# Performance work log

Measured on AMD Instinct MI355X. Metric: run time of the kernel, lower is better.

## Reference

```python
import jax, jax.numpy as jnp
import numpy as np

ALPHA = 0.5
SIGMA = 0.1
EPS = 1e-8
NUM_RISKS, B, T = 2, 8192, 64


def setup_inputs() -> dict:
    key = jax.random.key(0)
    k1, k2, k3, k4 = jax.random.split(key, 4)
    risk_outputs = jax.random.uniform(k1, (NUM_RISKS, B, T), dtype=jnp.float32)
    time_bins = jax.random.randint(k2, (B,), 0, T, dtype=jnp.int64)
    risk_indicators = jax.random.randint(k3, (B, NUM_RISKS), 0, 2).astype(bool)
    event_indicators = jax.random.randint(k4, (B,), 0, 2).astype(bool)
    return {
        "risk_outputs": risk_outputs,
        "time_bins": time_bins,
        "risk_indicators": risk_indicators,
        "event_indicators": event_indicators,
    }


def _deephit_loss(risk_outputs, time_bins, risk_indicators, event_indicators):
    ev = event_indicators  # (B,) bool: event occurred
    cens = ~ev             # (B,) bool: censored
    # pairwise mask M[i,j]: i censored, j had event, t_j <= t_i
    pair_mask = cens[:, None] & ev[None, :] & (time_bins[None, :] <= time_bins[:, None])

    def per_risk(pred, rind):
        # pred: (B, T), rind: (B,) bool
        # ---- likelihood: -mean(log p_i(t_i)) over samples with this risk's event
        probs = jnp.take_along_axis(pred, time_bins[:, None], axis=1)[:, 0]  # (B,)
        mask = rind & ev
        cnt = mask.sum()
        log_sum = jnp.where(mask, jnp.log(probs + EPS), 0.0).sum()
        ll = jnp.where(cnt > 0, -log_sum / jnp.maximum(cnt, 1).astype(pred.dtype), 0.0)
        # ---- ranking: sum sigmoid((F_i(t_i) - F_j(t_i)) / sigma) over valid (i,j) pairs
        cum = jnp.cumsum(pred, axis=1)          # (B, T)
        G = cum[:, time_bins].T                  # G[i, j] = cum[j, t_i]  -> (B, B)
        diff = jnp.diagonal(G)[:, None] - G      # cum[i,t_i] - cum[j,t_i]
        rl = jnp.where(pair_mask, jax.nn.sigmoid(diff / SIGMA), 0.0).sum()
        return ll, rl

    ll, rl = jax.vmap(per_risk)(risk_outputs, risk_indicators.T)
    return ALPHA * ll.sum() + (1.0 - ALPHA) * rl.sum()


def reference(risk_outputs, time_bins, risk_indicators, event_indicators):
    return _deephit_loss(risk_outputs, time_bins, risk_indicators, event_indicators)
```

## Files before the change

kernel.cpp:

```cpp
#include <hip/hip_runtime.h>
#include <math.h>


namespace {
constexpr int R  = 2;
constexpr int Bn = 8192;
constexpr int Tn = 64;
constexpr float INV_SIGMA = 10.0f;
constexpr float EPS       = 1e-8f;
}


__global__ void k_prep(const int* __restrict__ tb, const int* __restrict__ ev,
                       int* limE, int* cbase, int* ncensG,
                       int* esort, int* csort, int* accZero) {
    __shared__ int hE[Tn], hC[Tn], wE[Tn], wC[Tn];
    int tid = threadIdx.x;
    if (tid < Tn) { hE[tid] = 0; hC[tid] = 0; }
    if (tid < 192) accZero[tid] = 0;
    __syncthreads();
    for (int j = tid; j < Bn; j += 1024) {
        int t = tb[j];
        if (ev[j]) atomicAdd(&hE[t], 1);
        else       atomicAdd(&hC[t], 1);
    }
    __syncthreads();
    if (tid == 0) {
        int ae = 0, ac = 0;
        for (int t = 0; t < Tn; ++t) {
            wE[t] = ae; ae += hE[t]; limE[t] = ae;
            wC[t] = ac; cbase[t] = ac; ncensG[t] = hC[t]; ac += hC[t];
        }
    }
    __syncthreads();
    for (int j = tid; j < Bn; j += 1024) {
        int t = tb[j];
        if (ev[j]) { int p = atomicAdd(&wE[t], 1); esort[p] = j; }
        else       { int p = atomicAdd(&wC[t], 1); csort[p] = j; }
    }
}

__global__ void __launch_bounds__(256)
k_cum(const float* __restrict__ risk, const int* __restrict__ tb,
      const int* __restrict__ rind,
      const int* __restrict__ limE, const int* __restrict__ cbase,
      const int* __restrict__ ncens,
      const int* __restrict__ esort, const int* __restrict__ csort,
      float* __restrict__ cumTs, float* __restrict__ aCens,
      float* llsumArr, int* cntArr) {
    const int r    = blockIdx.y;
    const int lane = threadIdx.x & 63;
    const int w    = threadIdx.x >> 6;
    __shared__ float S[Tn][Tn + 1];
    __shared__ int idxS[Tn];

    if (blockIdx.x < 128) {
        int nE = limE[Tn - 1];
        int k0 = blockIdx.x * 64;
        if (k0 >= nE) return;
        int cnt = min(64, nE - k0);
        if (threadIdx.x < cnt) idxS[threadIdx.x] = esort[k0 + threadIdx.x];
        __syncthreads();
        for (int s = 0; s < 16; ++s) {
            int ls = w * 16 + s;
            if (ls < cnt) {
                int i = idxS[ls];
                float v = risk[((size_t)r * Bn + i) * Tn + lane];
                float c = v;
#pragma unroll
                for (int o = 1; o < 64; o <<= 1) {
                    float u = __shfl_up(c, o, 64);
                    if (lane >= o) c += u;
                }
                S[lane][ls] = c;
                int ti = tb[i];
                float p = __shfl(v, ti, 64);
                if (lane == 0 && rind[i * R + r]) {
                    int slot = r * 32 + ((k0 + ls) & 31);
                    atomicAdd(&llsumArr[slot], logf(p + EPS));
                    atomicAdd(&cntArr[slot], 1);
                }
            }
        }
        __syncthreads();
        float* dst = cumTs + ((size_t)r * Tn) * Bn + k0;
        int col = threadIdx.x & 63;
        int tr0 = threadIdx.x >> 6;
        if (col < cnt) {
#pragma unroll
            for (int m = 0; m < 16; ++m) {
                int t = m * 4 + tr0;
                dst[(size_t)t * Bn + col] = S[t][col];
            }
        }
    } else {
        int nC = cbase[Tn - 1] + ncens[Tn - 1];
        int k0 = (blockIdx.x - 128) * 64;
        if (k0 >= nC) return;
        int cnt = min(64, nC - k0);
        if (threadIdx.x < cnt) idxS[threadIdx.x] = csort[k0 + threadIdx.x];
        __syncthreads();
        for (int s = 0; s < 16; ++s) {
            int ls = w * 16 + s;
            if (ls < cnt) {
                int i  = idxS[ls];
                int ti = tb[i];
                float v = risk[((size_t)r * Bn + i) * Tn + lane];
                v = (lane <= ti) ? v : 0.f;
#pragma unroll
                for (int o = 32; o > 0; o >>= 1) v += __shfl_down(v, o, 64);
                if (lane == 0) aCens[r * Bn + k0 + ls] = v;
            }
        }
    }
}

__global__ void k_rank(const float* __restrict__ cumTs, const float* __restrict__ aCens,
                       const int* __restrict__ limE, const int* __restrict__ cbase,
                       const int* __restrict__ ncens, float* rlsumArr) {
    int t = blockIdx.z, r = blockIdx.y, ec = blockIdx.x;
    int ne = limE[t];
    if (ec * 1024 >= ne) return;
    int nc = ncens[t];
    if (nc == 0) return;

    int j0 = ec * 1024 + threadIdx.x * 4;
    const float* rowp = cumTs + ((size_t)(r * Tn + t)) * Bn;
    float4 c4 = *reinterpret_cast<const float4*>(rowp + j0);
    float c0 = (j0 + 0 < ne) ? c4.x * INV_SIGMA : INFINITY;
    float c1 = (j0 + 1 < ne) ? c4.y * INV_SIGMA : INFINITY;
    float c2 = (j0 + 2 < ne) ? c4.z * INV_SIGMA : INFINITY;
    float c3 = (j0 + 3 < ne) ? c4.w * INV_SIGMA : INFINITY;

    const float* aC = aCens + r * Bn + cbase[t];
    float s0 = 0.f, s1 = 0.f, s2 = 0.f, s3 = 0.f;
#pragma unroll 4
    for (int ii = 0; ii < nc; ++ii) {
        float a10 = aC[ii] * INV_SIGMA;
        s0 += __builtin_amdgcn_rcpf(1.f + __expf(c0 - a10));
        s1 += __builtin_amdgcn_rcpf(1.f + __expf(c1 - a10));
        s2 += __builtin_amdgcn_rcpf(1.f + __expf(c2 - a10));
        s3 += __builtin_amdgcn_rcpf(1.f + __expf(c3 - a10));
    }
    float s = (s0 + s1) + (s2 + s3);
#pragma unroll
    for (int o = 32; o > 0; o >>= 1) s += __shfl_down(s, o, 64);
    if ((threadIdx.x & 63) == 0) {
        int slot = r * 32 + ((blockIdx.z * 8 + blockIdx.x) & 31);
        atomicAdd(&rlsumArr[slot], s);
    }
}

__global__ void k_final(const float* llsumArr, const int* cntArr,
                        const float* rlsumArr, float* out) {
    int lane = threadIdx.x;
    float lg = llsumArr[lane];
    float rl = rlsumArr[lane];
    int   cn = cntArr[lane];
#pragma unroll
    for (int o = 1; o <= 16; o <<= 1) {
        lg += __shfl_xor(lg, o, 64);
        rl += __shfl_xor(rl, o, 64);
        cn += __shfl_xor(cn, o, 64);
    }
    float lg1 = __shfl(lg, 32, 64);
    float rl1 = __shfl(rl, 32, 64);
    int   cn1 = __shfl(cn, 32, 64);
    if (lane == 0) {
        float ll0 = (cn  > 0) ? (-lg  / (float)cn ) : 0.f;
        float ll1 = (cn1 > 0) ? (-lg1 / (float)cn1) : 0.f;
        out[0] = 0.5f * (ll0 + ll1) + 0.5f * (rl + rl1);
    }
}

extern "C" void kernel_launch(void* const* d_in, const int* in_sizes, int n_in,
                              void* d_out, int out_size, void* d_ws, size_t ws_size,
                              hipStream_t stream) {
    const float* risk = (const float*)d_in[0];
    const int* tb     = (const int*)d_in[1];
    const int* rind   = (const int*)d_in[2];
    const int* ev     = (const int*)d_in[3];

    char* ws = (char*)d_ws;
    float* llsumArr = (float*)(ws + 0);
    int*   cntArr   = (int*)(ws + 256);
    float* rlsumArr = (float*)(ws + 512);
    int*   limE     = (int*)(ws + 768);
    int*   cbase    = (int*)(ws + 1024);
    int*   ncens    = (int*)(ws + 1280);
    int*   esort    = (int*)(ws + 2048);
    int*   csort    = (int*)(ws + 34816);
    float* aCens    = (float*)(ws + 67584);
    float* cumTs    = (float*)(ws + 133120);

    k_prep<<<1, 1024, 0, stream>>>(tb, ev, limE, cbase, ncens, esort, csort,
                                   (int*)ws);
    dim3 gc(256, R);
    k_cum<<<gc, 256, 0, stream>>>(risk, tb, rind, limE, cbase, ncens,
                                  esort, csort, cumTs, aCens, llsumArr, cntArr);
    dim3 gr(8, R, Tn);
    k_rank<<<gr, 256, 0, stream>>>(cumTs, aCens, limE, cbase, ncens, rlsumArr);
    k_final<<<1, 64, 0, stream>>>(llsumArr, cntArr, rlsumArr, (float*)d_out);
}
```

Before: 116.8 us.

## Fuse all stages into one persistent kernel with software grid barriers

Replaces the four-kernel pipeline with a single persistent 256-block, 1024-thread kernel that uses atomic grid barriers between the histogram, scan, scatter, cumulative-sum and ranking stages. The histogram and scatter are now spread over 8 blocks instead of one, and the ranking work is split by (risk, time, half of the censored range) across all blocks. This targets launch overhead and the serial single-block prep kernel. In exchange it adds grid-barrier spin costs and a memset launch, and it relies on all 256 large blocks being co-resident, which can deadlock if that does not hold.

```diff
diff --git a/kernel.cpp b/kernel.cpp
--- a/kernel.cpp
+++ b/kernel.cpp
@@ -6,170 +6,228 @@
 constexpr int R  = 2;
 constexpr int Bn = 8192;
 constexpr int Tn = 64;
+constexpr int NB = 256;
+constexpr int NT = 1024;
 constexpr float INV_SIGMA = 10.0f;
 constexpr float EPS       = 1e-8f;
 }
 
 
-__global__ void k_prep(const int* __restrict__ tb, const int* __restrict__ ev,
-                       int* limE, int* cbase, int* ncensG,
-                       int* esort, int* csort, int* accZero) {
-    __shared__ int hE[Tn], hC[Tn], wE[Tn], wC[Tn];
-    int tid = threadIdx.x;
-    if (tid < Tn) { hE[tid] = 0; hC[tid] = 0; }
-    if (tid < 192) accZero[tid] = 0;
+__device__ __forceinline__ void gridbar(int* bar, int want) {
     __syncthreads();
-    for (int j = tid; j < Bn; j += 1024) {
+    if (threadIdx.x == 0) {
+        __threadfence();
+        int t = __hip_atomic_fetch_add(&bar[0], 1, __ATOMIC_ACQ_REL,
+                                       __HIP_MEMORY_SCOPE_AGENT);
+        if (t == NB - 1) {
+            __hip_atomic_store(&bar[0], 0, __ATOMIC_RELAXED,
+                               __HIP_MEMORY_SCOPE_AGENT);
+            __hip_atomic_fetch_add(&bar[1], 1, __ATOMIC_ACQ_REL,
+                                   __HIP_MEMORY_SCOPE_AGENT);
+        } else {
+            while (__hip_atomic_load(&bar[1], __ATOMIC_ACQUIRE,
+                                     __HIP_MEMORY_SCOPE_AGENT) < want) {
+                __builtin_amdgcn_s_sleep(2);
+            }
+        }
+        __threadfence();
+    }
+    __syncthreads();
+}
+
+__global__ void __launch_bounds__(NT)
+k_fused(const float* __restrict__ risk, const int* __restrict__ tb,
+        const int* __restrict__ rind, const int* __restrict__ ev,
+        float* __restrict__ out, int* __restrict__ wsI) {
+    float* llsumArr = (float*)(wsI + 0);
+    int*   cntArr   = wsI + 64;
+    float* rlsumArr = (float*)(wsI + 128);
+    int*   bar      = wsI + 192;
+    int*   binE     = wsI + 208;
+    int*   binC     = wsI + 272;
+    int*   limE     = wsI + 336;
+    int*   cbaseA   = wsI + 400;
+    int*   ncensA   = wsI + 464;
+    int*   scatE    = wsI + 528;
+    int*   scatC    = wsI + 592;
+    int*   esort    = wsI + 1024;
+    int*   csort    = wsI + 9216;
+    float* aCens    = (float*)(wsI + 17408);
+    float* cumTs    = (float*)(wsI + 33792);
+
+    const int b    = blockIdx.x;
+    const int tid  = threadIdx.x;
+    const int lane = tid & 63;
+    const int w    = tid >> 6;
+
+    __shared__ float S[Tn][Tn + 1];
+    __shared__ int idxS[Tn], tbS[Tn];
+    __shared__ int hE[Tn], hC[Tn];
+
+    if (b < 8) {
+        if (tid < Tn) { hE[tid] = 0; hC[tid] = 0; }
+        __syncthreads();
+        int j = b * 1024 + tid;
         int t = tb[j];
         if (ev[j]) atomicAdd(&hE[t], 1);
         else       atomicAdd(&hC[t], 1);
-    }
-    __syncthreads();
-    if (tid == 0) {
-        int ae = 0, ac = 0;
-        for (int t = 0; t < Tn; ++t) {
-            wE[t] = ae; ae += hE[t]; limE[t] = ae;
-            wC[t] = ac; cbase[t] = ac; ncensG[t] = hC[t]; ac += hC[t];
-        }
-    }
-    __syncthreads();
-    for (int j = tid; j < Bn; j += 1024) {
+        __syncthreads();
+        if (tid < Tn) {
+            if (hE[tid]) atomicAdd(&binE[tid], hE[tid]);
+            if (hC[tid]) atomicAdd(&binC[tid], hC[tid]);
+        }
+    }
+    gridbar(bar, 1);
+
+    if (b == 0 && tid < 64) {
+        int eC = binE[tid], cC = binC[tid];
+        int se = eC, sc = cC;
+#pragma unroll
+        for (int o = 1; o < 64; o <<= 1) {
+            int ue = __shfl_up(se, o, 64);
+            int uc = __shfl_up(sc, o, 64);
+            if (lane >= o) { se += ue; sc += uc; }
+        }
+        limE[tid]   = se;
+        scatE[tid]  = se - eC;
+        cbaseA[tid] = sc - cC;
+        scatC[tid]  = sc - cC;
+        ncensA[tid] = cC;
+    }
+    gridbar(bar, 2);
+
+    if (b < 8) {
+        int j = b * 1024 + tid;
         int t = tb[j];
-        if (ev[j]) { int p = atomicAdd(&wE[t], 1); esort[p] = j; }
-        else       { int p = atomicAdd(&wC[t], 1); csort[p] = j; }
-    }
-}
-
-__global__ void __launch_bounds__(256)
-k_cum(const float* __restrict__ risk, const int* __restrict__ tb,
-      const int* __restrict__ rind,
-      const int* __restrict__ limE, const int* __restrict__ cbase,
-      const int* __restrict__ ncens,
-      const int* __restrict__ esort, const int* __restrict__ csort,
-      float* __restrict__ cumTs, float* __restrict__ aCens,
-      float* llsumArr, int* cntArr) {
-    const int r    = blockIdx.y;
-    const int lane = threadIdx.x & 63;
-    const int w    = threadIdx.x >> 6;
-    __shared__ float S[Tn][Tn + 1];
-    __shared__ int idxS[Tn];
-
-    if (blockIdx.x < 128) {
-        int nE = limE[Tn - 1];
-        int k0 = blockIdx.x * 64;
-        if (k0 >= nE) return;
-        int cnt = min(64, nE - k0);
-        if (threadIdx.x < cnt) idxS[threadIdx.x] = esort[k0 + threadIdx.x];
-        __syncthreads();
-        for (int s = 0; s < 16; ++s) {
-            int ls = w * 16 + s;
-            if (ls < cnt) {
-                int i = idxS[ls];
-                float v = risk[((size_t)r * Bn + i) * Tn + lane];
-                float c = v;
-#pragma unroll
-                for (int o = 1; o < 64; o <<= 1) {
-                    float u = __shfl_up(c, o, 64);
-                    if (lane >= o) c += u;
+        if (ev[j]) { int p = atomicAdd(&scatE[t], 1); esort[p] = j; }
+        else       { int p = atomicAdd(&scatC[t], 1); csort[p] = j; }
+    }
+    gridbar(bar, 3);
+
+    int nE = limE[Tn - 1];
+    int nC = Bn - nE;
+    for (int c = b; c < 512; c += NB) {
+        bool isEvent = (c < 256);
+        int r  = (c >> 7) & 1;
+        int k0 = (c & 127) * 64;
+        int tot = isEvent ? nE : nC;
+        if (k0 < tot) {
+            int cnt = min(64, tot - k0);
+            if (tid < cnt) {
+                int i = isEvent ? esort[k0 + tid] : csort[k0 + tid];
+                idxS[tid] = i;
+                tbS[tid]  = tb[i];
+            }
+            __syncthreads();
+            if (isEvent) {
+#pragma unroll
+                for (int s = 0; s < 4; ++s) {
+                    int ls = s * 16 + w;
+                    if (ls < cnt) {
+                        int i = idxS[ls];
+                        float v = risk[((size_t)r * Bn + i) * Tn + lane];
+                        float cc = v;
+#pragma unroll
+                        for (int o = 1; o < 64; o <<= 1) {
+                            float u = __shfl_up(cc, o, 64);
+                            if (lane >= o) cc += u;
+                        }
+                        S[lane][ls] = cc;
+                        int ti = tbS[ls];
+                        float p = __shfl(v, ti, 64);
+                        if (lane == 0 && rind[i * R + r]) {
+                            int slot = r * 32 + ((k0 + ls) & 31);
+                            atomicAdd(&llsumArr[slot], logf(p + EPS));
+                            atomicAdd(&cntArr[slot], 1);
+                        }
+                    }
                 }
-                S[lane][ls] = c;
-                int ti = tb[i];
-                float p = __shfl(v, ti, 64);
-                if (lane == 0 && rind[i * R + r]) {
-                    int slot = r * 32 + ((k0 + ls) & 31);
-                    atomicAdd(&llsumArr[slot], logf(p + EPS));
-                    atomicAdd(&cntArr[slot], 1);
+                __syncthreads();
+                int col = tid & 63, tr0 = tid >> 6;
+                if (col < cnt) {
+                    float* dst = cumTs + ((size_t)r * Tn) * Bn + k0;
+#pragma unroll
+                    for (int m = 0; m < 4; ++m) {
+                        int t = m * 16 + tr0;
+                        dst[(size_t)t * Bn + col] = S[t][col];
+                    }
                 }
-            }
-        }
-        __syncthreads();
-        float* dst = cumTs + ((size_t)r * Tn) * Bn + k0;
-        int col = threadIdx.x & 63;
-        int tr0 = threadIdx.x >> 6;
-        if (col < cnt) {
-#pragma unroll
-            for (int m = 0; m < 16; ++m) {
-                int t = m * 4 + tr0;
-                dst[(size_t)t * Bn + col] = S[t][col];
-            }
-        }
-    } else {
-        int nC = cbase[Tn - 1] + ncens[Tn - 1];
-        int k0 = (blockIdx.x - 128) * 64;
-        if (k0 >= nC) return;
-        int cnt = min(64, nC - k0);
-        if (threadIdx.x < cnt) idxS[threadIdx.x] = csort[k0 + threadIdx.x];
-        __syncthreads();
-        for (int s = 0; s < 16; ++s) {
-            int ls = w * 16 + s;
-            if (ls < cnt) {
-                int i  = idxS[ls];
-                int ti = tb[i];
-                float v = risk[((size_t)r * Bn + i) * Tn + lane];
-                v = (lane <= ti) ? v : 0.f;
-#pragma unroll
-                for (int o = 32; o > 0; o >>= 1) v += __shfl_down(v, o, 64);
-                if (lane == 0) aCens[r * Bn + k0 + ls] = v;
-            }
-        }
-    }
-}
-
-__global__ void k_rank(const float* __restrict__ cumTs, const float* __restrict__ aCens,
-                       const int* __restrict__ limE, const int* __restrict__ cbase,
-                       const int* __restrict__ ncens, float* rlsumArr) {
-    int t = blockIdx.z, r = blockIdx.y, ec = blockIdx.x;
-    int ne = limE[t];
-    if (ec * 1024 >= ne) return;
-    int nc = ncens[t];
-    if (nc == 0) return;
-
-    int j0 = ec * 1024 + threadIdx.x * 4;
-    const float* rowp = cumTs + ((size_t)(r * Tn + t)) * Bn;
-    float4 c4 = *reinterpret_cast<const float4*>(rowp + j0);
-    float c0 = (j0 + 0 < ne) ? c4.x * INV_SIGMA : INFINITY;
-    float c1 = (j0 + 1 < ne) ? c4.y * INV_SIGMA : INFINITY;
-    float c2 = (j0 + 2 < ne) ? c4.z * INV_SIGMA : INFINITY;
-    float c3 = (j0 + 3 < ne) ? c4.w * INV_SIGMA : INFINITY;
-
-    const float* aC = aCens + r * Bn + cbase[t];
-    float s0 = 0.f, s1 = 0.f, s2 = 0.f, s3 = 0.f;
+                __syncthreads();
+            } else {
+#pragma unroll
+                for (int s = 0; s < 4; ++s) {
+                    int ls = s * 16 + w;
+                    if (ls < cnt) {
+                        int i  = idxS[ls];
+                        int ti = tbS[ls];
+                        float v = risk[((size_t)r * Bn + i) * Tn + lane];
+                        v = (lane <= ti) ? v : 0.f;
+#pragma unroll
+                        for (int o = 32; o > 0; o >>= 1) v += __shfl_down(v, o, 64);
+                        if (lane == 0) aCens[r * Bn + k0 + ls] = v;
+                    }
+                }
+                __syncthreads();
+            }
+        }
+    }
+    gridbar(bar, 4);
+
+    {
+        int r    = b >> 7;
+        int t    = (b >> 1) & 63;
+        int half = b & 1;
+        int ne = limE[t], nc = ncensA[t], cb = cbaseA[t];
+        float s = 0.f;
+        if (ne > 0 && nc > 0) {
+            int e0 = tid * 4;
+            const float* rowp = cumTs + ((size_t)(r * Tn + t)) * Bn;
+            float4 c4 = *reinterpret_cast<const float4*>(rowp + e0);
+            float c0 = (e0 + 0 < ne) ? c4.x * INV_SIGMA : INFINITY;
+            float c1 = (e0 + 1 < ne) ? c4.y * INV_SIGMA : INFINITY;
+            float c2 = (e0 + 2 < ne) ? c4.z * INV_SIGMA : INFINITY;
+            float c3 = (e0 + 3 < ne) ? c4.w * INV_SIGMA : INFINITY;
+            int lo = half ? (nc >> 1) : 0;
+            int hi = half ? nc : (nc >> 1);
+            const float* aC = aCens + r * Bn + cb;
+            float s0 = 0.f, s1 = 0.f, s2 = 0.f, s3 = 0.f;
 #pragma unroll 4
-    for (int ii = 0; ii < nc; ++ii) {
-        float a10 = aC[ii] * INV_SIGMA;
-        s0 += __builtin_amdgcn_rcpf(1.f + __expf(c0 - a10));
-        s1 += __builtin_amdgcn_rcpf(1.f + __expf(c1 - a10));
-        s2 += __builtin_amdgcn_rcpf(1.f + __expf(c2 - a10));
-        s3 += __builtin_amdgcn_rcpf(1.f + __expf(c3 - a10));
-    }
-    float s = (s0 + s1) + (s2 + s3);
-#pragma unroll
-    for (int o = 32; o > 0; o >>= 1) s += __shfl_down(s, o, 64);
-    if ((threadIdx.x & 63) == 0) {
-        int slot = r * 32 + ((blockIdx.z * 8 + blockIdx.x) & 31);
-        atomicAdd(&rlsumArr[slot], s);
-    }
-}
-
-__global__ void k_final(const float* llsumArr, const int* cntArr,
-                        const float* rlsumArr, float* out) {
-    int lane = threadIdx.x;
-    float lg = llsumArr[lane];
-    float rl = rlsumArr[lane];
-    int   cn = cntArr[lane];
-#pragma unroll
-    for (int o = 1; o <= 16; o <<= 1) {
-        lg += __shfl_xor(lg, o, 64);
-        rl += __shfl_xor(rl, o, 64);
-        cn += __shfl_xor(cn, o, 64);
-    }
-    float lg1 = __shfl(lg, 32, 64);
-    float rl1 = __shfl(rl, 32, 64);
-    int   cn1 = __shfl(cn, 32, 64);
-    if (lane == 0) {
-        float ll0 = (cn  > 0) ? (-lg  / (float)cn ) : 0.f;
-        float ll1 = (cn1 > 0) ? (-lg1 / (float)cn1) : 0.f;
-        out[0] = 0.5f * (ll0 + ll1) + 0.5f * (rl + rl1);
+            for (int ci = lo; ci < hi; ++ci) {
+                float a10 = aC[ci] * INV_SIGMA;
+                s0 += __builtin_amdgcn_rcpf(1.f + __expf(c0 - a10));
+                s1 += __builtin_amdgcn_rcpf(1.f + __expf(c1 - a10));
+                s2 += __builtin_amdgcn_rcpf(1.f + __expf(c2 - a10));
+                s3 += __builtin_amdgcn_rcpf(1.f + __expf(c3 - a10));
+            }
+            s = (s0 + s1) + (s2 + s3);
+        }
+#pragma unroll
+        for (int o = 32; o > 0; o >>= 1) s += __shfl_down(s, o, 64);
+        if (lane == 0) {
+            int r2 = b >> 7;
+            atomicAdd(&rlsumArr[r2 * 32 + ((b * 16 + w) & 31)], s);
+        }
+    }
+    gridbar(bar, 5);
+
+    if (b == 0 && tid < 64) {
+        float lg = llsumArr[tid];
+        float rl = rlsumArr[tid];
+        int   cn = cntArr[tid];
+#pragma unroll
+        for (int o = 1; o <= 16; o <<= 1) {
+            lg += __shfl_xor(lg, o, 64);
+            rl += __shfl_xor(rl, o, 64);
+            cn += __shfl_xor(cn, o, 64);
+        }
+        float lg1 = __shfl(lg, 32, 64);
+        float rl1 = __shfl(rl, 32, 64);
+        int   cn1 = __shfl(cn, 32, 64);
+        if (tid == 0) {
+            float ll0 = (cn  > 0) ? (-lg  / (float)cn ) : 0.f;
+            float ll1 = (cn1 > 0) ? (-lg1 / (float)cn1) : 0.f;
+            out[0] = 0.5f * (ll0 + ll1) + 0.5f * (rl + rl1);
+        }
     }
 }
 
@@ -181,24 +239,7 @@
     const int* rind   = (const int*)d_in[2];
     const int* ev     = (const int*)d_in[3];
 
-    char* ws = (char*)d_ws;
-    float* llsumArr = (float*)(ws + 0);
-    int*   cntArr   = (int*)(ws + 256);
-    float* rlsumArr = (float*)(ws + 512);
-    int*   limE     = (int*)(ws + 768);
-    int*   cbase    = (int*)(ws + 1024);
-    int*   ncens    = (int*)(ws + 1280);
-    int*   esort    = (int*)(ws + 2048);
-    int*   csort    = (int*)(ws + 34816);
-    float* aCens    = (float*)(ws + 67584);
-    float* cumTs    = (float*)(ws + 133120);
-
-    k_prep<<<1, 1024, 0, stream>>>(tb, ev, limE, cbase, ncens, esort, csort,
-                                   (int*)ws);
-    dim3 gc(256, R);
-    k_cum<<<gc, 256, 0, stream>>>(risk, tb, rind, limE, cbase, ncens,
-                                  esort, csort, cumTs, aCens, llsumArr, cntArr);
-    dim3 gr(8, R, Tn);
-    k_rank<<<gr, 256, 0, stream>>>(cumTs, aCens, limE, cbase, ncens, rlsumArr);
-    k_final<<<1, 64, 0, stream>>>(llsumArr, cntArr, rlsumArr, (float*)d_out);
-}
+    hipMemsetAsync(d_ws, 0, 336 * 4, stream);
+    k_fused<<<NB, NT, 0, stream>>>(risk, tb, rind, ev, (float*)d_out,
+                                   (int*)d_ws);
+}
```

New measurement: 254.3 us. +117.7%, slower.
